# Kernel optimization log

Hardware: AMD Instinct MI355X
Metric: run time of the kernel (lower is better)

## Reference

```python
import jax, jax.numpy as jnp
import numpy as np

N = 50000        # num nodes
E = 1_000_000    # num edges
F_IN = 256       # input feature dim
UNITS = 128      # hidden units
NUM_CLASSES = 40 # output classes
EPS = 1e-3       # Keras BatchNormalization default epsilon


def setup_inputs() -> dict:
    key = jax.random.key(0)
    ks = jax.random.split(key, 32)
    inp = {
        "x": jax.random.normal(ks[0], (N, F_IN), jnp.float32),
        "edge_index": jax.random.randint(ks[1], (2, E), 0, N, jnp.int32),
        "edge_weight": jax.random.uniform(ks[2], (E,), jnp.float32),
    }
    dims = [(F_IN, UNITS), (UNITS, UNITS), (UNITS, NUM_CLASSES)]
    ki = 3
    for li, (fi, fo) in enumerate(dims, 1):
        inp[f"w_gcn{li}"] = jax.random.normal(ks[ki], (fi, fo), jnp.float32) / np.sqrt(fi).astype(np.float32); ki += 1
        inp[f"w_self{li}"] = jax.random.normal(ks[ki], (fi, fo), jnp.float32) / np.sqrt(fi).astype(np.float32); ki += 1
        inp[f"b{li}"] = jnp.zeros((fo,), jnp.float32)
        inp[f"gamma{li}"] = 1.0 + 0.1 * jax.random.normal(ks[ki], (fo,), jnp.float32); ki += 1
        inp[f"beta{li}"] = 0.1 * jax.random.normal(ks[ki], (fo,), jnp.float32); ki += 1
        inp[f"mean{li}"] = 0.1 * jax.random.normal(ks[ki], (fo,), jnp.float32); ki += 1
        inp[f"var{li}"] = jnp.ones((fo,), jnp.float32)
    return inp


def _gcn_bs(h, src, dst, norm_w, w_gcn, w_self, b, gamma, beta, mean, var, act):
    # GCN aggregation: transform then gather->weight->scatter-sum
    hw = h @ w_gcn                                   # [N, out]
    msg = hw[src] * norm_w[:, None]                  # [E, out]
    agg = jax.ops.segment_sum(msg, dst, num_segments=N)
    out = agg + h @ w_self + b                       # self-loop dense + bias
    # BatchNorm (inference: moving stats)
    out = (out - mean) * jax.lax.rsqrt(var + EPS) * gamma + beta
    return act(out) if act is not None else out


def reference(x, edge_index, edge_weight,
              w_gcn1, w_self1, b1, gamma1, beta1, mean1, var1,
              w_gcn2, w_self2, b2, gamma2, beta2, mean2, var2,
              w_gcn3, w_self3, b3, gamma3, beta3, mean3, var3):
    src, dst = edge_index[0], edge_index[1]
    # symmetric GCN normalization (renorm=False: no added self loops)
    deg = jax.ops.segment_sum(edge_weight, dst, num_segments=N)
    dinv = jnp.where(deg > 0, jax.lax.rsqrt(jnp.where(deg > 0, deg, 1.0)), 0.0)
    norm_w = dinv[src] * edge_weight * dinv[dst]
    # inference: DropEdge and Dropout are identity
    h = _gcn_bs(x, src, dst, norm_w, w_gcn1, w_self1, b1, gamma1, beta1, mean1, var1, jax.nn.relu)
    h = _gcn_bs(h, src, dst, norm_w, w_gcn2, w_self2, b2, gamma2, beta2, mean2, var2, jax.nn.relu)
    h = _gcn_bs(h, src, dst, norm_w, w_gcn3, w_self3, b3, gamma3, beta3, mean3, var3, None)
    return h
```

## Files before the change

kernel.cpp:

```cpp
#include <hip/hip_runtime.h>
#include <hip/hip_bf16.h>

#define NN 50000
#define EE 1000000
static constexpr float EPSV = 1e-3f;
static constexpr float FIXSCALE = 16777216.f;

typedef __attribute__((ext_vector_type(8))) short short8;
typedef __attribute__((ext_vector_type(4))) float fx4;

__device__ inline float blo(unsigned u) { return __uint_as_float(u << 16); }
__device__ inline float bhi(unsigned u) { return __uint_as_float(u & 0xffff0000u); }
__device__ inline unsigned short f2b(float f) {
    __hip_bfloat16 h = __float2bfloat16(f);
    return *(unsigned short*)&h;
}
__device__ inline unsigned pack2(float a, float b) {
    return (unsigned)f2b(a) | ((unsigned)f2b(b) << 16);
}

__device__ inline void gload_lds16(const unsigned short* g, unsigned short* ldsbase) {
    __builtin_amdgcn_global_load_lds(
        (const __attribute__((address_space(1))) unsigned int*)(const void*)g,
        (__attribute__((address_space(3))) unsigned int*)(void*)ldsbase, 16, 0, 0);
}


__global__ void zero_kernel(float* p, int n) {
    int i = blockIdx.x * blockDim.x + threadIdx.x;
    if (i < n) p[i] = 0.f;
}

__global__ void cntdeg_kernel(const int* __restrict__ ei, const float* __restrict__ ew,
                              unsigned long long* __restrict__ cnt64) {
    int e = blockIdx.x * blockDim.x + threadIdx.x;
    if (e < EE) {
        int d = ei[EE + e];
        unsigned fx = __float2uint_rn(ew[e] * FIXSCALE);
        atomicAdd(&cnt64[d], 0x100000000ull | (unsigned long long)fx);
    }
}

__global__ __launch_bounds__(1024) void dinvsum_kernel(const uint2* __restrict__ cnt64,
                                                       float* __restrict__ dinv,
                                                       int* __restrict__ bsum) {
    __shared__ int s[1024];
    const int t = threadIdx.x;
    int idx = blockIdx.x * 1024 + t;
    uint2 cv = make_uint2(0u, 0u);
    if (idx < NN) cv = cnt64[idx];
    float deg = (float)cv.x * (1.f / FIXSCALE);
    if (idx < NN) dinv[idx] = (deg > 0.f) ? rsqrtf(deg) : 0.f;
    s[t] = (int)cv.y;
    __syncthreads();
#pragma unroll
    for (int off = 512; off > 0; off >>= 1) {
        if (t < off) s[t] += s[t + off];
        __syncthreads();
    }
    if (t == 0) bsum[blockIdx.x] = s[0];
}

__global__ __launch_bounds__(64) void scanB_kernel(const int* __restrict__ bsum,
                                                   int* __restrict__ bpre, int nb) {
    int t = threadIdx.x;
    int v = (t < nb) ? bsum[t] : 0;
    int own = v;
#pragma unroll
    for (int off = 1; off < 64; off <<= 1) {
        int u = __shfl_up(v, off);
        if (t >= off) v += u;
    }
    if (t < nb) bpre[t] = v - own;
}

__global__ __launch_bounds__(1024) void scanC_kernel(const uint2* __restrict__ cnt64,
                                                     const int* __restrict__ bpre,
                                                     int* __restrict__ rowstart) {
    __shared__ int s[1024];
    const int t = threadIdx.x;
    int idx = blockIdx.x * 1024 + t;
    int v = (idx < NN) ? (int)cnt64[idx].y : 0;
    s[t] = v;
    __syncthreads();
#pragma unroll
    for (int off = 1; off < 1024; off <<= 1) {
        int u = (t >= off) ? s[t - off] : 0;
        __syncthreads();
        s[t] += u;
        __syncthreads();
    }
    if (idx < NN) rowstart[idx] = s[t] - v + bpre[blockIdx.x];
    if (idx == 0) rowstart[NN] = EE;
}

__global__ void fill_kernel(const int* __restrict__ ei, const float* __restrict__ ew,
                            const float* __restrict__ dinv, const int* __restrict__ rowstart,
                            int* __restrict__ cnt2, uint2* __restrict__ eprec) {
    int e = blockIdx.x * blockDim.x + threadIdx.x;
    if (e >= EE) return;
    int s = ei[e], d = ei[EE + e];
    int idx = rowstart[d] + atomicAdd(&cnt2[d], 1);
    float w = dinv[s] * ew[e] * dinv[d];
    eprec[idx] = make_uint2((unsigned)s, __float_as_uint(w));
}


__global__ void xconv_kernel(const float4* __restrict__ x, uint2* __restrict__ xb, int n4) {
    int i = blockIdx.x * 256 + threadIdx.x;
    if (i < n4) {
        float4 v = x[i];
        xb[i] = make_uint2(pack2(v.x, v.y), pack2(v.z, v.w));
    }
}


__global__ void wconv_kernel(const float* __restrict__ Wg, const float* __restrict__ Ws,
                             unsigned short* __restrict__ Wt, int K, int Fo, int N2) {
    int idx = blockIdx.x * 256 + threadIdx.x;
    if (idx >= N2 * K) return;
    int n = idx / K, k = idx - n * K;
    float v = 0.f;
    if (n < Fo) v = Wg[(size_t)k * Fo + n];
    else if (n < 2 * Fo) v = Ws[(size_t)k * Fo + (n - Fo)];
    Wt[idx] = f2b(v);
}


__global__ __launch_bounds__(256) void gemm_mfma(const unsigned short* __restrict__ Ab,
                                                 const unsigned short* __restrict__ Wt,
                                                 const float* __restrict__ bias,
                                                 unsigned short* __restrict__ Cg,
                                                 unsigned short* __restrict__ Cs,
                                                 int M, int K, int Fo) {
    __shared__ unsigned short sA[128 * 64];
    __shared__ unsigned short sB[128 * 64];

    const int t = threadIdx.x;
    const int lane = t & 63;
    const int wave = t >> 6;
    const int wm = wave >> 1, wn = wave & 1;
    const int l15 = lane & 15, quad = lane >> 4;
    const int row0 = blockIdx.x * 128;
    const int colbase = blockIdx.y * 128;

    fx4 acc[4][4];
#pragma unroll
    for (int r = 0; r < 4; ++r)
#pragma unroll
        for (int c = 0; c < 4; ++c) acc[r][c] = (fx4){0.f, 0.f, 0.f, 0.f};

    for (int kc = 0; kc < K; kc += 64) {
#pragma unroll
        for (int j = 0; j < 4; ++j) {
            int c = wave * 4 + j;
            int rb = c >> 1, kh = c & 1;
            int ar = row0 + rb * 16 + l15;
            if (ar >= M) ar = M - 1;
            int ak = kc + kh * 32 + quad * 8;
            gload_lds16(Ab + (size_t)ar * K + ak, sA + c * 512);
            int br = colbase + rb * 16 + l15;
            gload_lds16(Wt + (size_t)br * K + ak, sB + c * 512);
        }
        __syncthreads();

#pragma unroll
        for (int kh = 0; kh < 2; ++kh) {
            short8 a[4], b[4];
#pragma unroll
            for (int r = 0; r < 4; ++r)
                a[r] = *reinterpret_cast<const short8*>(&sA[((wm * 4 + r) * 2 + kh) * 512 + lane * 8]);
#pragma unroll
            for (int c = 0; c < 4; ++c)
                b[c] = *reinterpret_cast<const short8*>(&sB[((wn * 4 + c) * 2 + kh) * 512 + lane * 8]);
#pragma unroll
            for (int r = 0; r < 4; ++r)
#pragma unroll
                for (int c = 0; c < 4; ++c)
                    acc[r][c] = __builtin_amdgcn_mfma_f32_16x16x32_bf16(a[r], b[c], acc[r][c], 0, 0, 0);
        }
        __syncthreads();
    }

#pragma unroll
    for (int c = 0; c < 4; ++c) {
        int f = colbase + wn * 64 + c * 16 + l15;
        if (f >= 2 * Fo) continue;
        bool isG = (f < Fo);
        int col = isG ? f : f - Fo;
        float badd = isG ? 0.f : bias[col];
        unsigned short* base = isG ? Cg : Cs;
#pragma unroll
        for (int r = 0; r < 4; ++r) {
#pragma unroll
            for (int reg = 0; reg < 4; ++reg) {
                int row = row0 + wm * 64 + r * 16 + quad * 4 + reg;
                if (row < M) base[(size_t)row * Fo + col] = f2b(acc[r][c][reg] + badd);
            }
        }
    }
}


template <bool RELU>
__global__ __launch_bounds__(256) void agg128_kernel(
    const int* __restrict__ rowstart, const uint2* __restrict__ eprec,
    const unsigned* __restrict__ hw, const unsigned* __restrict__ selfC,
    const float* __restrict__ g, const float* __restrict__ be,
    const float* __restrict__ mu, const float* __restrict__ va,
    unsigned* __restrict__ out) {
    int wave = threadIdx.x >> 6;
    int lane = threadIdx.x & 63;
    int n = blockIdx.x * 4 + wave;
    if (n >= NN) return;
    unsigned scp = selfC[n * 64 + lane];
    float acc0 = blo(scp), acc1 = bhi(scp);
    int beg = rowstart[n], end = rowstart[n + 1];
    int i = beg;
    for (; i + 4 <= end; i += 4) {
        uint2 e0 = eprec[i], e1 = eprec[i + 1], e2 = eprec[i + 2], e3 = eprec[i + 3];
        unsigned v0 = hw[e0.x * 64u + lane];
        unsigned v1 = hw[e1.x * 64u + lane];
        unsigned v2 = hw[e2.x * 64u + lane];
        unsigned v3 = hw[e3.x * 64u + lane];
        float w0 = __uint_as_float(e0.y), w1 = __uint_as_float(e1.y);
        float w2 = __uint_as_float(e2.y), w3 = __uint_as_float(e3.y);
        acc0 += blo(v0) * w0; acc1 += bhi(v0) * w0;
        acc0 += blo(v1) * w1; acc1 += bhi(v1) * w1;
        acc0 += blo(v2) * w2; acc1 += bhi(v2) * w2;
        acc0 += blo(v3) * w3; acc1 += bhi(v3) * w3;
    }
    for (; i < end; ++i) {
        uint2 e = eprec[i];
        unsigned v = hw[e.x * 64u + lane];
        float w = __uint_as_float(e.y);
        acc0 += blo(v) * w; acc1 += bhi(v) * w;
    }
    float2 m2 = reinterpret_cast<const float2*>(mu)[lane];
    float2 v2f = reinterpret_cast<const float2*>(va)[lane];
    float2 g2 = reinterpret_cast<const float2*>(g)[lane];
    float2 b2 = reinterpret_cast<const float2*>(be)[lane];
    float r0 = (acc0 - m2.x) * rsqrtf(v2f.x + EPSV) * g2.x + b2.x;
    float r1 = (acc1 - m2.y) * rsqrtf(v2f.y + EPSV) * g2.y + b2.y;
    if (RELU) {
        r0 = fmaxf(r0, 0.f);
        r1 = fmaxf(r1, 0.f);
    }
    out[n * 64 + lane] = pack2(r0, r1);
}


__global__ __launch_bounds__(256) void agg40_kernel(
    const int* __restrict__ rowstart, const uint2* __restrict__ eprec,
    const unsigned* __restrict__ hw, const unsigned* __restrict__ selfC,
    const float* __restrict__ g, const float* __restrict__ be,
    const float* __restrict__ mu, const float* __restrict__ va,
    float* __restrict__ out) {
    int wave = threadIdx.x >> 6;
    int lane = threadIdx.x & 63;
    int n = blockIdx.x * 4 + wave;
    if (n >= NN) return;
    int grp = lane / 20;
    int fl = lane - grp * 20;
    float acc0 = 0.f, acc1 = 0.f;
    int beg = rowstart[n], end = rowstart[n + 1];
    if (grp < 3) {
        for (int i = beg + grp; i < end; i += 3) {
            uint2 e = eprec[i];
            unsigned v = hw[e.x * 20u + fl];
            float w = __uint_as_float(e.y);
            acc0 += blo(v) * w;
            acc1 += bhi(v) * w;
        }
    }
    acc0 += __shfl(acc0, lane + 20) + __shfl(acc0, lane + 40);
    acc1 += __shfl(acc1, lane + 20) + __shfl(acc1, lane + 40);
    if (lane < 20) {
        int f0 = lane * 2;
        unsigned scp = selfC[n * 20 + lane];
        acc0 += blo(scp);
        acc1 += bhi(scp);
        float2 m2 = reinterpret_cast<const float2*>(mu)[lane];
        float2 v2f = reinterpret_cast<const float2*>(va)[lane];
        float2 g2 = reinterpret_cast<const float2*>(g)[lane];
        float2 b2 = reinterpret_cast<const float2*>(be)[lane];
        float r0 = (acc0 - m2.x) * rsqrtf(v2f.x + EPSV) * g2.x + b2.x;
        float r1 = (acc1 - m2.y) * rsqrtf(v2f.y + EPSV) * g2.y + b2.y;
        *reinterpret_cast<float2*>(&out[(size_t)n * 40 + f0]) = make_float2(r0, r1);
    }
}


extern "C" void kernel_launch(void* const* d_in, const int* in_sizes, int n_in,
                              void* d_out, int out_size, void* d_ws, size_t ws_size,
                              hipStream_t stream) {
    const float* x = (const float*)d_in[0];
    const int* ei = (const int*)d_in[1];
    const float* ew = (const float*)d_in[2];

    const float* wg[3]  = {(const float*)d_in[3],  (const float*)d_in[10], (const float*)d_in[17]};
    const float* wsf[3] = {(const float*)d_in[4],  (const float*)d_in[11], (const float*)d_in[18]};
    const float* bs[3]  = {(const float*)d_in[5],  (const float*)d_in[12], (const float*)d_in[19]};
    const float* gm[3]  = {(const float*)d_in[6],  (const float*)d_in[13], (const float*)d_in[20]};
    const float* bt[3]  = {(const float*)d_in[7],  (const float*)d_in[14], (const float*)d_in[21]};
    const float* mu[3]  = {(const float*)d_in[8],  (const float*)d_in[15], (const float*)d_in[22]};
    const float* vr[3]  = {(const float*)d_in[9],  (const float*)d_in[16], (const float*)d_in[23]};

    float* W = (float*)d_ws;
    unsigned long long* cnt64 = (unsigned long long*)W;
    float* dinv     = W + 100096;
    int*   cnt2     = (int*)(W + 150144);
    int*   bsum     = (int*)(W + 200192);
    int*   bpre     = (int*)(W + 200256);
    int*   rowstart = (int*)(W + 200320);
    uint2* eprec    = (uint2*)(W + 250432);
    unsigned short* Wt1 = (unsigned short*)(W + 2250432);
    unsigned short* Wt2 = (unsigned short*)(W + 2283200);
    unsigned short* Wt3 = (unsigned short*)(W + 2299584);
    unsigned short* xb  = (unsigned short*)(W + 2307776);
    unsigned short* bufH = (unsigned short*)(W + 2307776);
    unsigned short* bufHW = (unsigned short*)(W + 8707776);
    unsigned short* bufSb = (unsigned short*)(W + 11907776);

    const int B = 256;
    const int SB = 49;

    zero_kernel<<<(200192 + B - 1) / B, B, 0, stream>>>(W, 200192);
    cntdeg_kernel<<<(EE + B - 1) / B, B, 0, stream>>>(ei, ew, cnt64);
    dinvsum_kernel<<<SB, 1024, 0, stream>>>((const uint2*)cnt64, dinv, bsum);
    scanB_kernel<<<1, 64, 0, stream>>>(bsum, bpre, SB);
    scanC_kernel<<<SB, 1024, 0, stream>>>((const uint2*)cnt64, bpre, rowstart);
    fill_kernel<<<(EE + B - 1) / B, B, 0, stream>>>(ei, ew, dinv, rowstart, cnt2, eprec);

    xconv_kernel<<<(NN * 64 + B - 1) / B, B, 0, stream>>>((const float4*)x, (uint2*)xb, NN * 64);
    wconv_kernel<<<(256 * 256 + B - 1) / B, B, 0, stream>>>(wg[0], wsf[0], Wt1, 256, 128, 256);
    wconv_kernel<<<(256 * 128 + B - 1) / B, B, 0, stream>>>(wg[1], wsf[1], Wt2, 128, 128, 256);
    wconv_kernel<<<(128 * 128 + B - 1) / B, B, 0, stream>>>(wg[2], wsf[2], Wt3, 128, 40, 128);

    const int aggGrid = (NN + 3) / 4;
    dim3 g2((NN + 127) / 128, 2), g1((NN + 127) / 128, 1);

    gemm_mfma<<<g2, B, 0, stream>>>(xb, Wt1, bs[0], bufHW, bufSb, NN, 256, 128);
    agg128_kernel<true><<<aggGrid, B, 0, stream>>>(rowstart, eprec, (const unsigned*)bufHW,
                                                   (const unsigned*)bufSb, gm[0], bt[0], mu[0], vr[0],
                                                   (unsigned*)bufH);

    gemm_mfma<<<g2, B, 0, stream>>>(bufH, Wt2, bs[1], bufHW, bufSb, NN, 128, 128);
    agg128_kernel<true><<<aggGrid, B, 0, stream>>>(rowstart, eprec, (const unsigned*)bufHW,
                                                   (const unsigned*)bufSb, gm[1], bt[1], mu[1], vr[1],
                                                   (unsigned*)bufH);

    gemm_mfma<<<g1, B, 0, stream>>>(bufH, Wt3, bs[2], bufHW, bufSb, NN, 128, 40);
    agg40_kernel<<<aggGrid, B, 0, stream>>>(rowstart, eprec, (const unsigned*)bufHW,
                                            (const unsigned*)bufSb, gm[2], bt[2], mu[2], vr[2],
                                            (float*)d_out);
}
```

Baseline: 461.6 us.

## Reuse degree-atomic rank for CSR fill and pack edge records to 32 bits

```diff
diff --git a/kernel.cpp b/kernel.cpp
--- a/kernel.cpp
+++ b/kernel.cpp
@@ -32,12 +32,14 @@
 }
 
 __global__ void cntdeg_kernel(const int* __restrict__ ei, const float* __restrict__ ew,
-                              unsigned long long* __restrict__ cnt64) {
+                              unsigned long long* __restrict__ cnt64,
+                              unsigned* __restrict__ rank) {
     int e = blockIdx.x * blockDim.x + threadIdx.x;
     if (e < EE) {
         int d = ei[EE + e];
         unsigned fx = __float2uint_rn(ew[e] * FIXSCALE);
-        atomicAdd(&cnt64[d], 0x100000000ull | (unsigned long long)fx);
+        unsigned long long old = atomicAdd(&cnt64[d], 0x100000000ull | (unsigned long long)fx);
+        rank[e] = (unsigned)(old >> 32);
     }
 }
 
@@ -96,13 +98,13 @@
 
 __global__ void fill_kernel(const int* __restrict__ ei, const float* __restrict__ ew,
                             const float* __restrict__ dinv, const int* __restrict__ rowstart,
-                            int* __restrict__ cnt2, uint2* __restrict__ eprec) {
+                            const unsigned* __restrict__ rank, unsigned* __restrict__ eprec4) {
     int e = blockIdx.x * blockDim.x + threadIdx.x;
     if (e >= EE) return;
     int s = ei[e], d = ei[EE + e];
-    int idx = rowstart[d] + atomicAdd(&cnt2[d], 1);
+    int idx = rowstart[d] + (int)rank[e];
     float w = dinv[s] * ew[e] * dinv[d];
-    eprec[idx] = make_uint2((unsigned)s, __float_as_uint(w));
+    eprec4[idx] = ((unsigned)s << 16) | (unsigned)f2b(w);
 }
 
 
@@ -204,7 +206,7 @@
 
 template <bool RELU>
 __global__ __launch_bounds__(256) void agg128_kernel(
-    const int* __restrict__ rowstart, const uint2* __restrict__ eprec,
+    const int* __restrict__ rowstart, const unsigned* __restrict__ eprec4,
     const unsigned* __restrict__ hw, const unsigned* __restrict__ selfC,
     const float* __restrict__ g, const float* __restrict__ be,
     const float* __restrict__ mu, const float* __restrict__ va,
@@ -218,22 +220,21 @@
     int beg = rowstart[n], end = rowstart[n + 1];
     int i = beg;
     for (; i + 4 <= end; i += 4) {
-        uint2 e0 = eprec[i], e1 = eprec[i + 1], e2 = eprec[i + 2], e3 = eprec[i + 3];
-        unsigned v0 = hw[e0.x * 64u + lane];
-        unsigned v1 = hw[e1.x * 64u + lane];
-        unsigned v2 = hw[e2.x * 64u + lane];
-        unsigned v3 = hw[e3.x * 64u + lane];
-        float w0 = __uint_as_float(e0.y), w1 = __uint_as_float(e1.y);
-        float w2 = __uint_as_float(e2.y), w3 = __uint_as_float(e3.y);
+        unsigned e0 = eprec4[i], e1 = eprec4[i + 1], e2 = eprec4[i + 2], e3 = eprec4[i + 3];
+        unsigned v0 = hw[(e0 >> 16) * 64u + lane];
+        unsigned v1 = hw[(e1 >> 16) * 64u + lane];
+        unsigned v2 = hw[(e2 >> 16) * 64u + lane];
+        unsigned v3 = hw[(e3 >> 16) * 64u + lane];
+        float w0 = blo(e0), w1 = blo(e1), w2 = blo(e2), w3 = blo(e3);
         acc0 += blo(v0) * w0; acc1 += bhi(v0) * w0;
         acc0 += blo(v1) * w1; acc1 += bhi(v1) * w1;
         acc0 += blo(v2) * w2; acc1 += bhi(v2) * w2;
         acc0 += blo(v3) * w3; acc1 += bhi(v3) * w3;
     }
     for (; i < end; ++i) {
-        uint2 e = eprec[i];
-        unsigned v = hw[e.x * 64u + lane];
-        float w = __uint_as_float(e.y);
+        unsigned e = eprec4[i];
+        unsigned v = hw[(e >> 16) * 64u + lane];
+        float w = blo(e);
         acc0 += blo(v) * w; acc1 += bhi(v) * w;
     }
     float2 m2 = reinterpret_cast<const float2*>(mu)[lane];
@@ -251,7 +252,7 @@
 
 
 __global__ __launch_bounds__(256) void agg40_kernel(
-    const int* __restrict__ rowstart, const uint2* __restrict__ eprec,
+    const int* __restrict__ rowstart, const unsigned* __restrict__ eprec4,
     const unsigned* __restrict__ hw, const unsigned* __restrict__ selfC,
     const float* __restrict__ g, const float* __restrict__ be,
     const float* __restrict__ mu, const float* __restrict__ va,
@@ -266,9 +267,9 @@
     int beg = rowstart[n], end = rowstart[n + 1];
     if (grp < 3) {
         for (int i = beg + grp; i < end; i += 3) {
-            uint2 e = eprec[i];
-            unsigned v = hw[e.x * 20u + fl];
-            float w = __uint_as_float(e.y);
+            unsigned e = eprec4[i];
+            unsigned v = hw[(e >> 16) * 20u + fl];
+            float w = blo(e);
             acc0 += blo(v) * w;
             acc1 += bhi(v) * w;
         }
@@ -309,28 +310,28 @@
     float* W = (float*)d_ws;
     unsigned long long* cnt64 = (unsigned long long*)W;
     float* dinv     = W + 100096;
-    int*   cnt2     = (int*)(W + 150144);
-    int*   bsum     = (int*)(W + 200192);
-    int*   bpre     = (int*)(W + 200256);
-    int*   rowstart = (int*)(W + 200320);
-    uint2* eprec    = (uint2*)(W + 250432);
-    unsigned short* Wt1 = (unsigned short*)(W + 2250432);
-    unsigned short* Wt2 = (unsigned short*)(W + 2283200);
-    unsigned short* Wt3 = (unsigned short*)(W + 2299584);
-    unsigned short* xb  = (unsigned short*)(W + 2307776);
-    unsigned short* bufH = (unsigned short*)(W + 2307776);
-    unsigned short* bufHW = (unsigned short*)(W + 8707776);
-    unsigned short* bufSb = (unsigned short*)(W + 11907776);
+    unsigned* rank  = (unsigned*)(W + 150144);
+    int*   bsum     = (int*)(W + 1150144);
+    int*   bpre     = (int*)(W + 1150208);
+    int*   rowstart = (int*)(W + 1150272);
+    unsigned* eprec4 = (unsigned*)(W + 1200384);
+    unsigned short* Wt1 = (unsigned short*)(W + 2200384);
+    unsigned short* Wt2 = (unsigned short*)(W + 2233152);
+    unsigned short* Wt3 = (unsigned short*)(W + 2249536);
+    unsigned short* xb  = (unsigned short*)(W + 2257728);
+    unsigned short* bufH = (unsigned short*)(W + 2257728);
+    unsigned short* bufHW = (unsigned short*)(W + 8657728);
+    unsigned short* bufSb = (unsigned short*)(W + 11857728);
 
     const int B = 256;
     const int SB = 49;
 
-    zero_kernel<<<(200192 + B - 1) / B, B, 0, stream>>>(W, 200192);
-    cntdeg_kernel<<<(EE + B - 1) / B, B, 0, stream>>>(ei, ew, cnt64);
+    zero_kernel<<<(100096 + B - 1) / B, B, 0, stream>>>(W, 100096);
+    cntdeg_kernel<<<(EE + B - 1) / B, B, 0, stream>>>(ei, ew, cnt64, rank);
     dinvsum_kernel<<<SB, 1024, 0, stream>>>((const uint2*)cnt64, dinv, bsum);
     scanB_kernel<<<1, 64, 0, stream>>>(bsum, bpre, SB);
     scanC_kernel<<<SB, 1024, 0, stream>>>((const uint2*)cnt64, bpre, rowstart);
-    fill_kernel<<<(EE + B - 1) / B, B, 0, stream>>>(ei, ew, dinv, rowstart, cnt2, eprec);
+    fill_kernel<<<(EE + B - 1) / B, B, 0, stream>>>(ei, ew, dinv, rowstart, rank, eprec4);
 
     xconv_kernel<<<(NN * 64 + B - 1) / B, B, 0, stream>>>((const float4*)x, (uint2*)xb, NN * 64);
     wconv_kernel<<<(256 * 256 + B - 1) / B, B, 0, stream>>>(wg[0], wsf[0], Wt1, 256, 128, 256);
@@ -341,17 +342,17 @@
     dim3 g2((NN + 127) / 128, 2), g1((NN + 127) / 128, 1);
 
     gemm_mfma<<<g2, B, 0, stream>>>(xb, Wt1, bs[0], bufHW, bufSb, NN, 256, 128);
-    agg128_kernel<true><<<aggGrid, B, 0, stream>>>(rowstart, eprec, (const unsigned*)bufHW,
+    agg128_kernel<true><<<aggGrid, B, 0, stream>>>(rowstart, eprec4, (const unsigned*)bufHW,
                                                    (const unsigned*)bufSb, gm[0], bt[0], mu[0], vr[0],
                                                    (unsigned*)bufH);
 
     gemm_mfma<<<g2, B, 0, stream>>>(bufH, Wt2, bs[1], bufHW, bufSb, NN, 128, 128);
-    agg128_kernel<true><<<aggGrid, B, 0, stream>>>(rowstart, eprec, (const unsigned*)bufHW,
+    agg128_kernel<true><<<aggGrid, B, 0, stream>>>(rowstart, eprec4, (const unsigned*)bufHW,
                                                    (const unsigned*)bufSb, gm[1], bt[1], mu[1], vr[1],
                                                    (unsigned*)bufH);
 
     gemm_mfma<<<g1, B, 0, stream>>>(bufH, Wt3, bs[2], bufHW, bufSb, NN, 128, 40);
-    agg40_kernel<<<aggGrid, B, 0, stream>>>(rowstart, eprec, (const unsigned*)bufHW,
+    agg40_kernel<<<aggGrid, B, 0, stream>>>(rowstart, eprec4, (const unsigned*)bufHW,
                                             (const unsigned*)bufSb, gm[2], bt[2], mu[2], vr[2],
                                             (float*)d_out);
 }
```

New measurement: 432.5 us. 6.3% less time.
